# Kernel tuning notes

Hardware: AMD Instinct MI355X
Metric: run time of the kernel (lower is better)

The kernel has to match this reference:

```python
import jax, jax.numpy as jnp
import numpy as np

BITS = 4
GROUPSIZE = 128
IN_FEATURES = 4096
OUT_FEATURES = 4096
GROUPS = IN_FEATURES // GROUPSIZE  # 32
TOKENS = 8192


def setup_inputs() -> dict:
    key = jax.random.key(0)
    k_x, k_s, k_b = jax.random.split(key, 3)
    rng = np.random.default_rng(0)
    # packed 4-bit weights: 8 nibbles per int32 word
    qweight = jnp.asarray(
        rng.integers(-2**31, 2**31, size=(IN_FEATURES // 8, OUT_FEATURES), dtype=np.int64).astype(np.int32)
    )
    qzeros = jnp.asarray(
        rng.integers(-2**31, 2**31, size=(GROUPS, OUT_FEATURES // 8), dtype=np.int64).astype(np.int32)
    )
    scales = jax.random.uniform(k_s, (GROUPS, OUT_FEATURES), dtype=jnp.float32) * 0.02 + 0.001
    g_idx = (jnp.arange(IN_FEATURES, dtype=jnp.int32) // GROUPSIZE).astype(jnp.int32)
    bias = jax.random.normal(k_b, (OUT_FEATURES,), dtype=jnp.float32) * 0.01
    x = jax.random.normal(k_x, (TOKENS, IN_FEATURES), dtype=jnp.float32)
    return {"x": x, "qweight": qweight, "qzeros": qzeros, "scales": scales,
            "g_idx": g_idx, "bias": bias}


def reference(x, qweight, qzeros, scales, g_idx, bias):
    out_features = qweight.shape[1]
    in_features = qweight.shape[0] * 8
    mask = jnp.int32(15)  # 2**bits - 1
    wf = jnp.arange(0, 32, BITS, dtype=jnp.int32)  # [8] nibble shift amounts
    # unpack zero points: [groups, out//8, 8] -> [groups, out]
    zeros = ((qzeros[:, :, None] >> wf[None, None, :]) & mask) + 1
    zeros = zeros.reshape(scales.shape)
    # unpack weights: [in//8, 8, out] -> [in, out]
    weight = (qweight[:, None, :] >> wf[None, :, None]) & mask
    weight = weight.reshape(in_features, out_features)
    # dequantize per group and matmul
    W = scales[g_idx] * (weight - zeros[g_idx]).astype(scales.dtype)
    out = x @ W
    return out + bias
```

## Files before the change

### kernel.cpp

```cpp
#include <hip/hip_runtime.h>
#include <cstdint>
#include <cstddef>

#define IN_F   4096
#define OUT_F  4096
#define NTOK   8192
#define NGRP   32

#define BM 128
#define BN 128
#define BK 32

typedef __attribute__((ext_vector_type(8))) __bf16 bf16x8;
typedef __attribute__((ext_vector_type(4))) float  floatx4;

__device__ __forceinline__ unsigned short f2bf(float f) {
    unsigned int u = __builtin_bit_cast(unsigned int, f);
    u += 0x7fffu + ((u >> 16) & 1u);
    return (unsigned short)(u >> 16);
}

__device__ __forceinline__ void gload16(const void* g, void* l) {
    __builtin_amdgcn_global_load_lds(
        (const __attribute__((address_space(1))) void*)g,
        (__attribute__((address_space(3))) void*)l,
        16, 0, 0);
}

__global__ void dequant_kernel(const int* __restrict__ qweight,
                               const int* __restrict__ qzeros,
                               const float* __restrict__ scales,
                               const int* __restrict__ g_idx,
                               unsigned short* __restrict__ Wt) {
    __shared__ unsigned short tile[256 * 64];
    const int tk  = blockIdx.x & 63;
    const int tn  = blockIdx.x >> 6;
    const int tid = threadIdx.x;
    const int n   = tn * 256 + tid;

#pragma unroll
    for (int r = 0; r < 8; ++r) {
        const int k8 = tk * 8 + r;
        const int k  = k8 * 8;
        const int g  = g_idx[k];
        const int qw = qweight[(size_t)k8 * OUT_F + n];
        const float s = scales[g * OUT_F + n];
        const int  zw = qzeros[g * (OUT_F / 8) + (n >> 3)];
        const float z = (float)(((zw >> (4 * (n & 7))) & 15) + 1);
        const float sz = s * z;
        union { unsigned short h[8]; uint4 v; } u;
#pragma unroll
        for (int j = 0; j < 8; ++j)
            u.h[j] = f2bf(s * (float)((qw >> (4 * j)) & 15) - sz);
        *(uint4*)(tile + tid * 64 + ((r ^ (tid & 7)) * 8)) = u.v;
    }
    __syncthreads();
#pragma unroll
    for (int i = 0; i < 8; ++i) {
        const int nl = i * 32 + (tid >> 3);
        const int c  = tid & 7;
        const uint4 v = *(const uint4*)(tile + nl * 64 + ((c ^ (nl & 7)) * 8));
        *(uint4*)(Wt + (size_t)(tn * 256 + nl) * IN_F + tk * 64 + c * 8) = v;
    }
}

__global__ void xcast_kernel(const float* __restrict__ x,
                             unsigned short* __restrict__ Xb) {
    const size_t i = ((size_t)blockIdx.x * 256 + threadIdx.x) * 8;
    const float4 a = *(const float4*)(x + i);
    const float4 b = *(const float4*)(x + i + 4);
    union { unsigned short h[8]; uint4 v; } u;
    u.h[0] = f2bf(a.x); u.h[1] = f2bf(a.y); u.h[2] = f2bf(a.z); u.h[3] = f2bf(a.w);
    u.h[4] = f2bf(b.x); u.h[5] = f2bf(b.y); u.h[6] = f2bf(b.z); u.h[7] = f2bf(b.w);
    *(uint4*)(Xb + i) = u.v;
}

__global__ void gemm_kernel(const unsigned short* __restrict__ Xb,
                            const unsigned short* __restrict__ Wt,
                            const float* __restrict__ bias,
                            float* __restrict__ out) {
    __shared__ unsigned short As[BM * BK];
    __shared__ unsigned short Bs[BN * BK];

    const int tid  = threadIdx.x;
    const int wave = tid >> 6;
    const int lane = tid & 63;
    const int wm   = (wave >> 1) * 64;
    const int wn   = (wave & 1) * 64;
    const int m0   = blockIdx.y * BM;
    const int n0   = blockIdx.x * BN;

    const int sr   = lane >> 2;
    const int sc   = lane & 3;
    const int gch  = sc ^ ((sr >> 1) & 3);

    const int mi = lane & 15;
    const int kq = lane >> 4;
    const int swz = (mi >> 1) & 3;

    floatx4 acc[4][4];
#pragma unroll
    for (int i = 0; i < 4; ++i)
#pragma unroll
        for (int j = 0; j < 4; ++j)
            acc[i][j] = floatx4{0.f, 0.f, 0.f, 0.f};

    const unsigned short* Ag = Xb + (size_t)m0 * IN_F;
    const unsigned short* Bg = Wt + (size_t)n0 * IN_F;

    for (int k0 = 0; k0 < IN_F; k0 += BK) {
        __syncthreads();
#pragma unroll
        for (int c = 0; c < 2; ++c) {
            const int q   = wave * 2 + c;
            const int row = q * 16 + sr;
            gload16(Ag + (size_t)row * IN_F + k0 + gch * 8, (void*)(As + q * 16 * BK));
            gload16(Bg + (size_t)row * IN_F + k0 + gch * 8, (void*)(Bs + q * 16 * BK));
        }
        __syncthreads();

        bf16x8 av[4], bv[4];
#pragma unroll
        for (int i = 0; i < 4; ++i)
            av[i] = *(const bf16x8*)(As + (wm + i * 16 + mi) * BK + ((kq ^ swz) * 8));
#pragma unroll
        for (int j = 0; j < 4; ++j)
            bv[j] = *(const bf16x8*)(Bs + (wn + j * 16 + mi) * BK + ((kq ^ swz) * 8));
#pragma unroll
        for (int i = 0; i < 4; ++i)
#pragma unroll
            for (int j = 0; j < 4; ++j)
                acc[i][j] = __builtin_amdgcn_mfma_f32_16x16x32_bf16(
                    av[i], bv[j], acc[i][j], 0, 0, 0);
    }

    const int mq = lane >> 4;
#pragma unroll
    for (int j = 0; j < 4; ++j) {
        const int col = n0 + wn + j * 16 + mi;
        const float bb = bias[col];
#pragma unroll
        for (int i = 0; i < 4; ++i) {
#pragma unroll
            for (int r = 0; r < 4; ++r) {
                const int row = m0 + wm + i * 16 + mq * 4 + r;
                out[(size_t)row * OUT_F + col] = acc[i][j][r] + bb;
            }
        }
    }
}

extern "C" void kernel_launch(void* const* d_in, const int* in_sizes, int n_in,
                              void* d_out, int out_size, void* d_ws, size_t ws_size,
                              hipStream_t stream) {
    const float* x       = (const float*)d_in[0];
    const int*   qweight = (const int*)d_in[1];
    const int*   qzeros  = (const int*)d_in[2];
    const float* scales  = (const float*)d_in[3];
    const int*   g_idx   = (const int*)d_in[4];
    const float* bias    = (const float*)d_in[5];
    float*       out     = (float*)d_out;

    unsigned short* Wt = (unsigned short*)d_ws;
    unsigned short* Xb = Wt + (size_t)OUT_F * IN_F;

    dequant_kernel<<<64 * 16, 256, 0, stream>>>(qweight, qzeros, scales, g_idx, Wt);
    xcast_kernel<<<((size_t)NTOK * IN_F / 8) / 256, 256, 0, stream>>>(x, Xb);

    dim3 grid(OUT_F / BN, NTOK / BM);
    gemm_kernel<<<grid, 256, 0, stream>>>(Xb, Wt, bias, out);
}
```

Before: 537.7 us.

## Rewrite bf16 GEMM with 256x256x64 tiles, double-buffered LDS and interleaved loads

The GEMM kernel moves to 256x256 output tiles with BK=64 and 512 threads (8 waves of 128x64 each). It double-buffers LDS, issuing global-to-LDS loads for the next k-tile between MFMA quadrants, with manual vmcnt waits, barriers and s_setprio. It also adds a block-index swizzle for L2 locality. The goal is to hide global load latency behind MFMA work and raise arithmetic intensity per tile. The cost is much more register pressure (128 accumulator floats per thread) and fragile hand-written waitcnt and barrier ordering.

```diff
diff --git a/kernel.cpp b/kernel.cpp
--- a/kernel.cpp
+++ b/kernel.cpp
@@ -7,9 +7,11 @@
 #define NTOK   8192
 #define NGRP   32
 
-#define BM 128
-#define BN 128
-#define BK 32
+#define BM 256
+#define BN 256
+#define BK 64
+#define KTILES   (IN_F / BK)
+#define LDS_TILE (BM * BK)
 
 typedef __attribute__((ext_vector_type(8))) __bf16 bf16x8;
 typedef __attribute__((ext_vector_type(4))) float  floatx4;
@@ -75,75 +77,187 @@
     *(uint4*)(Xb + i) = u.v;
 }
 
-__global__ void gemm_kernel(const unsigned short* __restrict__ Xb,
-                            const unsigned short* __restrict__ Wt,
-                            const float* __restrict__ bias,
-                            float* __restrict__ out) {
-    __shared__ unsigned short As[BM * BK];
-    __shared__ unsigned short Bs[BN * BK];
+#define VMCNT4() asm volatile("s_waitcnt vmcnt(4)" ::: "memory")
+#define VMCNT2() asm volatile("s_waitcnt vmcnt(2)" ::: "memory")
+#define VMCNT0() asm volatile("s_waitcnt vmcnt(0)" ::: "memory")
+#define BARRIER() do { __builtin_amdgcn_s_barrier(); asm volatile("" ::: "memory"); } while (0)
+
+template<int I0, int J0>
+__device__ __forceinline__ void quad(floatx4 (&acc)[8][4],
+                                     const bf16x8 (&av)[4][2],
+                                     const bf16x8 (&bv)[4][2]) {
+#pragma unroll
+    for (int i4 = 0; i4 < 4; ++i4)
+#pragma unroll
+        for (int jj = 0; jj < 2; ++jj)
+#pragma unroll
+            for (int kk = 0; kk < 2; ++kk)
+                acc[I0 + i4][J0 + jj] = __builtin_amdgcn_mfma_f32_16x16x32_bf16(
+                    av[i4][kk], bv[J0 + jj][kk], acc[I0 + i4][J0 + jj], 0, 0, 0);
+}
+
+__global__ __launch_bounds__(512, 2) void gemm_kernel(
+        const unsigned short* __restrict__ Xb,
+        const unsigned short* __restrict__ Wt,
+        const float* __restrict__ bias,
+        float* __restrict__ out) {
+    __shared__ unsigned short As[2 * LDS_TILE];
+    __shared__ unsigned short Bs[2 * LDS_TILE];
 
     const int tid  = threadIdx.x;
     const int wave = tid >> 6;
     const int lane = tid & 63;
-    const int wm   = (wave >> 1) * 64;
-    const int wn   = (wave & 1) * 64;
-    const int m0   = blockIdx.y * BM;
-    const int n0   = blockIdx.x * BN;
-
-    const int sr   = lane >> 2;
-    const int sc   = lane & 3;
-    const int gch  = sc ^ ((sr >> 1) & 3);
-
-    const int mi = lane & 15;
-    const int kq = lane >> 4;
-    const int swz = (mi >> 1) & 3;
-
-    floatx4 acc[4][4];
-#pragma unroll
-    for (int i = 0; i < 4; ++i)
+    const int mi   = lane & 15;
+    const int kq   = lane >> 4;
+
+    const int bid = blockIdx.x;
+    const int swz = (bid & 7) * 64 + (bid >> 3);
+    const int m0  = (swz >> 4) * BM;
+    const int n0  = (swz & 15) * BN;
+
+    const int wrow = (wave >> 2) * 128;
+    const int wcol = (wave & 3) * 64;
+
+    const int lrow   = lane >> 3;
+    const int lchunk = ((lane & 7) ^ lrow) * 8;
+    const unsigned short* aSrc = Xb + (size_t)(m0 + lrow) * IN_F + lchunk;
+    const unsigned short* bSrc = Wt + (size_t)(n0 + lrow) * IN_F + lchunk;
+
+    const int raA = (wave >> 2) * 128 + (wave & 3) * 16;
+    const int raB = (wave >> 1) * 64  + (wave & 1) * 16;
+
+    const int aRd = (wrow + mi) * BK;
+    const int bRd = (wcol + mi) * BK;
+    const int cp0 = ((kq)     ^ (mi & 7)) * 8;
+    const int cp1 = ((4 + kq) ^ (mi & 7)) * 8;
+
+    floatx4 acc[8][4];
+#pragma unroll
+    for (int i = 0; i < 8; ++i)
 #pragma unroll
         for (int j = 0; j < 4; ++j)
             acc[i][j] = floatx4{0.f, 0.f, 0.f, 0.f};
 
-    const unsigned short* Ag = Xb + (size_t)m0 * IN_F;
-    const unsigned short* Bg = Wt + (size_t)n0 * IN_F;
-
-    for (int k0 = 0; k0 < IN_F; k0 += BK) {
-        __syncthreads();
-#pragma unroll
-        for (int c = 0; c < 2; ++c) {
-            const int q   = wave * 2 + c;
-            const int row = q * 16 + sr;
-            gload16(Ag + (size_t)row * IN_F + k0 + gch * 8, (void*)(As + q * 16 * BK));
-            gload16(Bg + (size_t)row * IN_F + k0 + gch * 8, (void*)(Bs + q * 16 * BK));
-        }
-        __syncthreads();
-
-        bf16x8 av[4], bv[4];
-#pragma unroll
-        for (int i = 0; i < 4; ++i)
-            av[i] = *(const bf16x8*)(As + (wm + i * 16 + mi) * BK + ((kq ^ swz) * 8));
-#pragma unroll
-        for (int j = 0; j < 4; ++j)
-            bv[j] = *(const bf16x8*)(Bs + (wn + j * 16 + mi) * BK + ((kq ^ swz) * 8));
-#pragma unroll
-        for (int i = 0; i < 4; ++i)
-#pragma unroll
-            for (int j = 0; j < 4; ++j)
-                acc[i][j] = __builtin_amdgcn_mfma_f32_16x16x32_bf16(
-                    av[i], bv[j], acc[i][j], 0, 0, 0);
-    }
-
-    const int mq = lane >> 4;
+    bf16x8 av[4][2], bv[4][2];
+
+    auto stageA = [&](int bufofs, int h, int kt) {
+        const int r0 = raA + h * 64;
+        gload16(aSrc + (size_t)(r0 + 0) * IN_F + (size_t)kt * BK,
+                (void*)(As + bufofs + (r0 + 0) * BK));
+        gload16(aSrc + (size_t)(r0 + 8) * IN_F + (size_t)kt * BK,
+                (void*)(As + bufofs + (r0 + 8) * BK));
+    };
+    auto stageB = [&](int bufofs, int h, int kt) {
+        const int r0 = raB + h * 32;
+        gload16(bSrc + (size_t)(r0 + 0) * IN_F + (size_t)kt * BK,
+                (void*)(Bs + bufofs + (r0 + 0) * BK));
+        gload16(bSrc + (size_t)(r0 + 8) * IN_F + (size_t)kt * BK,
+                (void*)(Bs + bufofs + (r0 + 8) * BK));
+    };
+    auto ldah = [&](int bufofs, int ah) {
+#pragma unroll
+        for (int i4 = 0; i4 < 4; ++i4) {
+            av[i4][0] = *(const bf16x8*)(As + bufofs + aRd + (ah * 4 + i4) * (16 * BK) + cp0);
+            av[i4][1] = *(const bf16x8*)(As + bufofs + aRd + (ah * 4 + i4) * (16 * BK) + cp1);
+        }
+    };
+    auto ldb01 = [&](int bufofs) {
+#pragma unroll
+        for (int jj = 0; jj < 2; ++jj) {
+            bv[jj][0] = *(const bf16x8*)(Bs + bufofs + bRd + jj * (16 * BK) + cp0);
+            bv[jj][1] = *(const bf16x8*)(Bs + bufofs + bRd + jj * (16 * BK) + cp1);
+        }
+    };
+    auto ldb23 = [&](int bufofs) {
+#pragma unroll
+        for (int jj = 0; jj < 2; ++jj) {
+            bv[2 + jj][0] = *(const bf16x8*)(Bs + bufofs + bRd + (2 + jj) * (16 * BK) + cp0);
+            bv[2 + jj][1] = *(const bf16x8*)(Bs + bufofs + bRd + (2 + jj) * (16 * BK) + cp1);
+        }
+    };
+
+    stageA(0, 0, 0);
+    stageB(0, 0, 0);
+    stageB(0, 1, 0);
+    stageA(0, 1, 0);
+    VMCNT4();
+    BARRIER();
+
+    for (int kt = 0; kt < KTILES - 1; ++kt) {
+        const int bo = (kt & 1) * LDS_TILE;
+        const int no = bo ^ LDS_TILE;
+        const int kn = kt + 1;
+
+        ldah(bo, 0); ldb01(bo);
+        stageA(no, 0, kn);
+        VMCNT4();
+        BARRIER();
+        __builtin_amdgcn_s_setprio(1);
+        quad<0, 0>(acc, av, bv);
+        __builtin_amdgcn_s_setprio(0);
+        BARRIER();
+
+        ldb23(bo);
+        stageB(no, 0, kn);
+        VMCNT4();
+        BARRIER();
+        __builtin_amdgcn_s_setprio(1);
+        quad<0, 2>(acc, av, bv);
+        __builtin_amdgcn_s_setprio(0);
+        BARRIER();
+
+        ldah(bo, 1);
+        stageB(no, 1, kn);
+        BARRIER();
+        __builtin_amdgcn_s_setprio(1);
+        quad<4, 2>(acc, av, bv);
+        __builtin_amdgcn_s_setprio(0);
+        BARRIER();
+
+        stageA(no, 1, kn);
+        VMCNT4();
+        BARRIER();
+        __builtin_amdgcn_s_setprio(1);
+        quad<4, 0>(acc, av, bv);
+        __builtin_amdgcn_s_setprio(0);
+        BARRIER();
+    }
+
+    {
+        const int bo = ((KTILES - 1) & 1) * LDS_TILE;
+        ldah(bo, 0); ldb01(bo);
+        VMCNT2();
+        BARRIER();
+        __builtin_amdgcn_s_setprio(1);
+        quad<0, 0>(acc, av, bv);
+        __builtin_amdgcn_s_setprio(0);
+        BARRIER();
+
+        ldb23(bo);
+        VMCNT0();
+        BARRIER();
+        __builtin_amdgcn_s_setprio(1);
+        quad<0, 2>(acc, av, bv);
+        __builtin_amdgcn_s_setprio(0);
+        BARRIER();
+
+        ldah(bo, 1);
+        __builtin_amdgcn_s_setprio(1);
+        quad<4, 2>(acc, av, bv);
+        quad<4, 0>(acc, av, bv);
+        __builtin_amdgcn_s_setprio(0);
+    }
+
+    const int mq = kq;
 #pragma unroll
     for (int j = 0; j < 4; ++j) {
-        const int col = n0 + wn + j * 16 + mi;
+        const int col = n0 + wcol + j * 16 + mi;
         const float bb = bias[col];
 #pragma unroll
-        for (int i = 0; i < 4; ++i) {
+        for (int i = 0; i < 8; ++i) {
 #pragma unroll
             for (int r = 0; r < 4; ++r) {
-                const int row = m0 + wm + i * 16 + mq * 4 + r;
+                const int row = m0 + wrow + i * 16 + mq * 4 + r;
                 out[(size_t)row * OUT_F + col] = acc[i][j][r] + bb;
             }
         }
@@ -167,6 +281,5 @@
     dequant_kernel<<<64 * 16, 256, 0, stream>>>(qweight, qzeros, scales, g_idx, Wt);
     xcast_kernel<<<((size_t)NTOK * IN_F / 8) / 256, 256, 0, stream>>>(x, Xb);
 
-    dim3 grid(OUT_F / BN, NTOK / BM);
-    gemm_kernel<<<grid, 256, 0, stream>>>(Xb, Wt, bias, out);
-}
+    gemm_kernel<<<dim3((NTOK / BM) * (OUT_F / BN)), 512, 0, stream>>>(Xb, Wt, bias, out);
+}
```

New measurement: 507.7 us. 1.06x faster.
